# Kernel optimization log

Hardware: AMD Instinct MI355X
Metric: run time of the kernel (lower is better)

The kernel has to match this reference:

```python
import jax, jax.numpy as jnp
import numpy as np

DICT_SIZE = 512
EMBED_DIM = 64
SPARSITY = 5
COMMITMENT_COST = 0.25
EPSILON = 1e-10
COEFF_CLAMP = 1e7


def setup_inputs() -> dict:
    key = jax.random.key(0)
    kz, kd = jax.random.split(key)
    z = jax.random.normal(kz, (32, EMBED_DIM, 32, 32), dtype=jnp.float32)
    D = jax.random.normal(kd, (EMBED_DIM, DICT_SIZE), dtype=jnp.float32)
    # _normalize_dictionary(): unit L2 norm per atom (column)
    D = D / jnp.linalg.norm(D, axis=0, keepdims=True)
    return {"z": z, "dictionary": D}


def batch_omp(signals, dictionary):
    # signals: [E, N], dictionary: [E, K]
    E, N = signals.shape
    K = dictionary.shape[1]
    Dt = dictionary.T  # [K, E]
    DtD = Dt @ dictionary + EPSILON * jnp.eye(K, dtype=signals.dtype)  # [K, K]
    residual = signals
    active = jnp.zeros((N, K), dtype=bool)
    coefficients = jnp.zeros((N, K), dtype=signals.dtype)
    idx = jnp.zeros((N, 0), dtype=jnp.int32)
    rows = jnp.arange(N)
    for k in range(SPARSITY):  # small fixed unroll; active-set size is static k+1
        corr = Dt @ residual                                  # [K, N]
        corr = jnp.where(active.T, -jnp.inf, corr)
        new_atoms = jnp.argmax(corr, axis=0).astype(jnp.int32)  # [N]
        active = active.at[rows, new_atoms].set(True)
        idx = jnp.concatenate([idx, new_atoms[:, None]], axis=1)  # [N, k+1]
        G = DtD[idx[:, :, None], idx[:, None, :]]             # [N, k+1, k+1]
        y = jnp.einsum('nke,en->nk', Dt[idx], residual)       # [N, k+1]
        coeffs = jnp.linalg.solve(G, y[..., None])[..., 0]    # [N, k+1]
        update = jnp.einsum('enk,nk->en', dictionary[:, idx], coeffs)  # [E, N]
        residual = signals - update
        coefficients = coefficients.at[rows[:, None], idx].set(coeffs)
    return coefficients.T  # [K, N]


def reference(z, dictionary):
    B, E, H, W = z.shape
    # [B,E,H,W] -> [E, N]
    z_flat = z.transpose(0, 2, 3, 1).reshape(-1, E).T
    # sparse coding is done under no_grad in torch
    coefficients = jax.lax.stop_gradient(batch_omp(z_flat, dictionary))
    coefficients = jnp.clip(coefficients, -COEFF_CLAMP, COEFF_CLAMP)  # [K, N]
    z_q_flat = dictionary @ coefficients                               # [E, N]
    z_q_reshaped = z_q_flat.T.reshape(B, H, W, E).transpose(0, 3, 1, 2)
    rec_loss = jnp.mean((jax.lax.stop_gradient(z_q_flat) - z_flat) ** 2)
    commit_loss = jnp.mean((z_q_flat - jax.lax.stop_gradient(z_flat)) ** 2)
    effective_cost = COMMITMENT_COST * (1.0 + SPARSITY / 10.0)
    coeff_loss = jnp.mean(jnp.abs(coefficients))
    loss = rec_loss + effective_cost * commit_loss + 0.001 * coeff_loss
    # straight-through estimator with clamp
    z_q = z + jax.lax.stop_gradient(jnp.clip(z_q_reshaped - z, -1.0, 1.0))
    return z_q, loss, coefficients
```

## Files before the change

kernel.cpp:

```cpp
#include <hip/hip_runtime.h>
#include <math.h>

#define NSIG 32768
#define KD   512
#define ED   64
#define SP   5

__global__ __launch_bounds__(256) void k_dtd(const float* __restrict__ D,
                                             double* __restrict__ DtD) {
  int flat = blockIdx.x * 256 + threadIdx.x;
  int i = flat >> 9, j = flat & 511;
  double acc = 0.0;
  #pragma unroll
  for (int e = 0; e < ED; ++e)
    acc += (double)D[e * KD + i] * (double)D[e * KD + j];
  if (i == j) acc += 1e-10;
  DtD[flat] = acc;
}

__global__ __launch_bounds__(256) void k_zero(float4* __restrict__ p, size_t count4) {
  size_t i = (size_t)blockIdx.x * 256 + threadIdx.x;
  size_t stride = (size_t)gridDim.x * 256;
  float4 zv = make_float4(0.f, 0.f, 0.f, 0.f);
  for (; i < count4; i += stride) p[i] = zv;
}

template <int K>
__device__ __forceinline__ void omp_iter(const double* __restrict__ DtD,
                                         const double (&c0)[16], unsigned& amask,
                                         int (&idx)[SP], double (&cc)[SP],
                                         double (&tri)[15], double (&c0sel)[SP],
                                         int li) {
  double vb = -INFINITY;
  int ab = 0x7FFFFFFF;
  #pragma unroll
  for (int j4 = 0; j4 < 4; ++j4) {
    int a0 = (j4 << 7) + (li << 2);
    double v0 = c0[4 * j4], v1 = c0[4 * j4 + 1];
    double v2 = c0[4 * j4 + 2], v3 = c0[4 * j4 + 3];
    #pragma unroll
    for (int m = 0; m < K; ++m) {
      const double* gp = DtD + (size_t)idx[m] * KD + a0;
      double2 gA = *(const double2*)gp;
      double2 gB = *(const double2*)(gp + 2);
      v0 -= gA.x * cc[m];
      v1 -= gA.y * cc[m];
      v2 -= gB.x * cc[m];
      v3 -= gB.y * cc[m];
    }
    v0 = ((amask >> (4 * j4 + 0)) & 1u) ? -INFINITY : v0;
    v1 = ((amask >> (4 * j4 + 1)) & 1u) ? -INFINITY : v1;
    v2 = ((amask >> (4 * j4 + 2)) & 1u) ? -INFINITY : v2;
    v3 = ((amask >> (4 * j4 + 3)) & 1u) ? -INFINITY : v3;
    if (v0 > vb) { vb = v0; ab = a0; }
    if (v1 > vb) { vb = v1; ab = a0 + 1; }
    if (v2 > vb) { vb = v2; ab = a0 + 2; }
    if (v3 > vb) { vb = v3; ab = a0 + 3; }
  }
  #pragma unroll
  for (int s = 16; s >= 1; s >>= 1) {
    double ov = __shfl_xor(vb, s, 64);
    int    oa = __shfl_xor(ab, s, 64);
    if (ov > vb || (ov == vb && oa < ab)) { vb = ov; ab = oa; }
  }
  idx[K] = ab;
  if (((ab >> 2) & 31) == li) amask |= 1u << ((((ab >> 7) << 2)) | (ab & 3));
  const double* drow = DtD + (size_t)ab * KD;
  double bb[SP], u[SP];
  #pragma unroll
  for (int m = 0; m < K; ++m) bb[m] = drow[idx[m]];
  {
    double csel = vb;
    #pragma unroll
    for (int m = 0; m < K; ++m) csel += bb[m] * cc[m];
    c0sel[K] = csel;
  }
  double sch = drow[ab];
  #pragma unroll
  for (int i = 0; i < K; ++i) {
    double ui = 0.0;
    #pragma unroll
    for (int m = 0; m < K; ++m) {
      int lo = i < m ? i : m, hi = i < m ? m : i;
      ui += tri[lo * SP - lo * (lo + 1) / 2 + hi] * bb[m];
    }
    u[i] = ui;
    sch -= bb[i] * ui;
  }
  double r = 1.0 / sch;
  #pragma unroll
  for (int i = 0; i < K; ++i) {
    #pragma unroll
    for (int j = i; j < K; ++j) tri[i * SP - i * (i + 1) / 2 + j] += r * u[i] * u[j];
    tri[i * SP - i * (i + 1) / 2 + K] = -r * u[i];
  }
  tri[K * SP - K * (K + 1) / 2 + K] = r;
  double h[SP];
  #pragma unroll
  for (int i = 0; i <= K; ++i) {
    double s = 0.0;
    #pragma unroll
    for (int j = 0; j <= K; ++j) {
      int lo = i < j ? i : j, hi = i < j ? j : i;
      s += tri[lo * SP - lo * (lo + 1) / 2 + hi] * c0sel[j];
    }
    h[i] = s;
  }
  #pragma unroll
  for (int i = 0; i < K; ++i) cc[i] = h[i] - cc[i];
  cc[K] = h[K];
}

__device__ __forceinline__ void corr_phase(const float* __restrict__ z,
                                           const float* __restrict__ D,
                                           float* __restrict__ Dlds,
                                           float* __restrict__ zbuf,
                                           int tid, int li, int mysig,
                                           int blockId, double (&c0)[16]) {
  int n = blockId * 8 + mysig;
  int b = n >> 10, p0 = (blockId * 8) & 1023;
  {
    const float* zb = z + (size_t)b * 65536 + p0;
    #pragma unroll
    for (int k2 = 0; k2 < 2; ++k2) {
      int f = tid + 256 * k2;
      zbuf[f] = zb[(f >> 3) * 1024 + (f & 7)];
    }
  }
  #pragma unroll
  for (int j = 0; j < 16; ++j) c0[j] = 0.0;
  for (int t4 = 0; t4 < 4; ++t4) {
    __syncthreads();
    {
      const float4* src = (const float4*)(D + t4 * 16 * 512);
      float4* dst = (float4*)Dlds;
      #pragma unroll
      for (int i = 0; i < 8; ++i) dst[tid + 256 * i] = src[tid + 256 * i];
    }
    __syncthreads();
    #pragma unroll 4
    for (int e = 0; e < 16; ++e) {
      double zv = (double)zbuf[(t4 * 16 + e) * 8 + mysig];
      const float* drow = Dlds + e * 512;
      #pragma unroll
      for (int j4 = 0; j4 < 4; ++j4) {
        float4 dv = *(const float4*)(drow + (j4 << 7) + (li << 2));
        c0[4 * j4 + 0] += zv * (double)dv.x;
        c0[4 * j4 + 1] += zv * (double)dv.y;
        c0[4 * j4 + 2] += zv * (double)dv.z;
        c0[4 * j4 + 3] += zv * (double)dv.w;
      }
    }
  }
}

__global__ __launch_bounds__(256) void k_fused(const float* __restrict__ z,
                                               const float* __restrict__ D,
                                               const double* __restrict__ DtD,
                                               float* __restrict__ coefOut,
                                               int* __restrict__ idxWs,
                                               double* __restrict__ cWs,
                                               double* __restrict__ csumWs) {
  __shared__ float Dlds[16 * 512];
  __shared__ float zbuf[64 * 8];
  int tid = threadIdx.x;
  int li = tid & 31;
  int mysig = ((tid >> 6) << 1) | ((tid >> 5) & 1);
  int n = blockIdx.x * 8 + mysig;
  double c0[16];
  corr_phase(z, D, Dlds, zbuf, tid, li, mysig, blockIdx.x, c0);
  unsigned amask = 0;
  int idx[SP]; double cc[SP]; double tri[15]; double c0sel[SP];
  omp_iter<0>(DtD, c0, amask, idx, cc, tri, c0sel, li);
  omp_iter<1>(DtD, c0, amask, idx, cc, tri, c0sel, li);
  omp_iter<2>(DtD, c0, amask, idx, cc, tri, c0sel, li);
  omp_iter<3>(DtD, c0, amask, idx, cc, tri, c0sel, li);
  omp_iter<4>(DtD, c0, amask, idx, cc, tri, c0sel, li);
  if (li == 0) {
    double cs = 0.0;
    #pragma unroll
    for (int j = 0; j < SP; ++j) {
      double cj = cc[j];
      cj = fmin(fmax(cj, -10000000.0), 10000000.0);
      cs += fabs(cj);
      idxWs[n * SP + j] = idx[j];
      cWs[n * SP + j] = cj;
      coefOut[(size_t)idx[j] * NSIG + n] = (float)cj;
    }
    csumWs[n] = cs;
  }
}

__global__ __launch_bounds__(256) void k_corr_probe(const float* __restrict__ z,
                                                    const float* __restrict__ D,
                                                    double* __restrict__ probeWs) {
  __shared__ float Dlds[16 * 512];
  __shared__ float zbuf[64 * 8];
  int tid = threadIdx.x;
  int li = tid & 31;
  int mysig = ((tid >> 6) << 1) | ((tid >> 5) & 1);
  double c0[16];
  corr_phase(z, D, Dlds, zbuf, tid, li, mysig, blockIdx.x, c0);
  double s = 0.0;
  #pragma unroll
  for (int j = 0; j < 16; ++j) s += c0[j];
  if (s == 12345.6789012345) probeWs[blockIdx.x] = s;
}

__global__ __launch_bounds__(256) void k_zq(const float* __restrict__ z,
                                            const float* __restrict__ D,
                                            const int* __restrict__ idxWs,
                                            const double* __restrict__ cWs,
                                            float* __restrict__ zqOut,
                                            double* __restrict__ recWs) {
  int t = threadIdx.x;
  size_t flat = (size_t)blockIdx.x * 256 + t;
  int b = (int)(flat >> 16);
  int e = (int)((flat >> 10) & 63);
  int p = (int)(flat & 1023);
  int n = b * 1024 + p;
  double u = 0.0;
  #pragma unroll
  for (int j = 0; j < SP; ++j) {
    int a = idxWs[n * SP + j];
    u += (double)D[e * KD + a] * cWs[n * SP + j];
  }
  float zv = z[flat];
  double d = u - (double)zv;
  double dc = fmin(fmax(d, -1.0), 1.0);
  zqOut[flat] = (float)((double)zv + dc);
  __shared__ double red[256];
  red[t] = d * d;
  __syncthreads();
  #pragma unroll
  for (int s = 128; s >= 1; s >>= 1) {
    if (t < s) red[t] += red[t + s];
    __syncthreads();
  }
  if (t == 0) recWs[blockIdx.x] = red[0];
}

__global__ __launch_bounds__(256) void k_loss(const double* __restrict__ recWs,
                                              const double* __restrict__ csumWs,
                                              float* __restrict__ lossOut) {
  int t = threadIdx.x;
  double r = 0.0, c = 0.0;
  for (int i = t; i < 8192; i += 256) r += recWs[i];
  for (int i = t; i < NSIG; i += 256) c += csumWs[i];
  __shared__ double red[512];
  red[t] = r; red[256 + t] = c;
  __syncthreads();
  #pragma unroll
  for (int s = 128; s >= 1; s >>= 1) {
    if (t < s) { red[t] += red[t + s]; red[256 + t] += red[256 + t + s]; }
    __syncthreads();
  }
  if (t == 0) {
    double rec = red[0] / (double)(64.0 * 32768.0);
    double cm  = red[256] / (double)(512.0 * 32768.0);
    double loss = rec + 0.375 * rec + 0.001 * cm;
    lossOut[0] = (float)loss;
  }
}

extern "C" void kernel_launch(void* const* d_in, const int* in_sizes, int n_in,
                              void* d_out, int out_size, void* d_ws, size_t ws_size,
                              hipStream_t stream) {
  const float* z = (const float*)d_in[0];
  const float* D = (const float*)d_in[1];
  float* out = (float*)d_out;
  float* zqOut   = out;
  float* lossOut = out + 2097152;
  float* coefOut = out + 2097153;

  char* w = (char*)d_ws;
  double* DtD    = (double*)w; w += (size_t)KD * KD * 8;
  int*    idxWs  = (int*)w;    w += (size_t)NSIG * SP * 4;
  double* cWs    = (double*)w; w += (size_t)NSIG * SP * 8;
  double* csumWs = (double*)w; w += (size_t)NSIG * 8;
  double* recWs  = (double*)w; w += (size_t)8192 * 8;
  double* probeWs = (double*)w; w += (size_t)4096 * 8;

  k_dtd<<<1024, 256, 0, stream>>>(D, DtD);
  k_zero<<<2048, 256, 0, stream>>>((float4*)coefOut, (size_t)KD * NSIG / 4);
  k_fused<<<NSIG / 8, 256, 0, stream>>>(z, D, DtD, coefOut, idxWs, cWs, csumWs);
  k_zq<<<8192, 256, 0, stream>>>(z, D, idxWs, cWs, zqOut, recWs);
  k_loss<<<1, 256, 0, stream>>>(recWs, csumWs, lossOut);
  k_corr_probe<<<2048, 256, 0, stream>>>(z, D, probeWs);
}
```

Before: 263.3 us.

## Compute two signals per wave in correlation phase and drop probe kernel

The correlation phase is restructured so each 64-lane wave computes correlations for two signals at once. Each lane reads 8 contiguous dictionary atoms from LDS and reuses them for both signals, which halves LDS reads per FMA. The results are then redistributed with shuffles back into the per-half-wave layout the OMP iterations expect. The separate probe kernel that reran the correlation phase is also removed, eliminating a full extra launch's worth of work.

Result: faster. 229.3 us (-12.9%).

```diff
diff --git a/kernel.cpp b/kernel.cpp
--- a/kernel.cpp
+++ b/kernel.cpp
@@ -109,49 +109,6 @@
   #pragma unroll
   for (int i = 0; i < K; ++i) cc[i] = h[i] - cc[i];
   cc[K] = h[K];
-}
-
-__device__ __forceinline__ void corr_phase(const float* __restrict__ z,
-                                           const float* __restrict__ D,
-                                           float* __restrict__ Dlds,
-                                           float* __restrict__ zbuf,
-                                           int tid, int li, int mysig,
-                                           int blockId, double (&c0)[16]) {
-  int n = blockId * 8 + mysig;
-  int b = n >> 10, p0 = (blockId * 8) & 1023;
-  {
-    const float* zb = z + (size_t)b * 65536 + p0;
-    #pragma unroll
-    for (int k2 = 0; k2 < 2; ++k2) {
-      int f = tid + 256 * k2;
-      zbuf[f] = zb[(f >> 3) * 1024 + (f & 7)];
-    }
-  }
-  #pragma unroll
-  for (int j = 0; j < 16; ++j) c0[j] = 0.0;
-  for (int t4 = 0; t4 < 4; ++t4) {
-    __syncthreads();
-    {
-      const float4* src = (const float4*)(D + t4 * 16 * 512);
-      float4* dst = (float4*)Dlds;
-      #pragma unroll
-      for (int i = 0; i < 8; ++i) dst[tid + 256 * i] = src[tid + 256 * i];
-    }
-    __syncthreads();
-    #pragma unroll 4
-    for (int e = 0; e < 16; ++e) {
-      double zv = (double)zbuf[(t4 * 16 + e) * 8 + mysig];
-      const float* drow = Dlds + e * 512;
-      #pragma unroll
-      for (int j4 = 0; j4 < 4; ++j4) {
-        float4 dv = *(const float4*)(drow + (j4 << 7) + (li << 2));
-        c0[4 * j4 + 0] += zv * (double)dv.x;
-        c0[4 * j4 + 1] += zv * (double)dv.y;
-        c0[4 * j4 + 2] += zv * (double)dv.z;
-        c0[4 * j4 + 3] += zv * (double)dv.w;
-      }
-    }
-  }
 }
 
 __global__ __launch_bounds__(256) void k_fused(const float* __restrict__ z,
@@ -164,11 +121,67 @@
   __shared__ float Dlds[16 * 512];
   __shared__ float zbuf[64 * 8];
   int tid = threadIdx.x;
-  int li = tid & 31;
-  int mysig = ((tid >> 6) << 1) | ((tid >> 5) & 1);
-  int n = blockIdx.x * 8 + mysig;
+  int lane = tid & 63;
+  int wv = tid >> 6;
+  int li = lane & 31;
+  int g  = lane >> 5;
+  int n = blockIdx.x * 8 + 2 * wv + g;
+  {
+    int n0 = blockIdx.x * 8;
+    int b = n0 >> 10, p0 = n0 & 1023;
+    const float* zb = z + (size_t)b * 65536 + p0;
+    #pragma unroll
+    for (int k2 = 0; k2 < 2; ++k2) {
+      int f = tid + 256 * k2;
+      zbuf[f] = zb[(f >> 3) * 1024 + (f & 7)];
+    }
+  }
+  double cA[8], cB[8];
+  #pragma unroll
+  for (int p = 0; p < 8; ++p) { cA[p] = 0.0; cB[p] = 0.0; }
+  for (int t4 = 0; t4 < 4; ++t4) {
+    __syncthreads();
+    {
+      const float4* src = (const float4*)(D + t4 * 16 * 512);
+      float4* dst = (float4*)Dlds;
+      #pragma unroll
+      for (int i = 0; i < 8; ++i) dst[tid + 256 * i] = src[tid + 256 * i];
+    }
+    __syncthreads();
+    #pragma unroll 4
+    for (int e = 0; e < 16; ++e) {
+      float2 zz = *(const float2*)(zbuf + (t4 * 16 + e) * 8 + 2 * wv);
+      double zA = (double)zz.x, zB = (double)zz.y;
+      const float* dp = Dlds + e * 512 + lane * 8;
+      float4 d0 = *(const float4*)dp;
+      float4 d1 = *(const float4*)(dp + 4);
+      double dv[8] = {(double)d0.x, (double)d0.y, (double)d0.z, (double)d0.w,
+                      (double)d1.x, (double)d1.y, (double)d1.z, (double)d1.w};
+      #pragma unroll
+      for (int p = 0; p < 8; ++p) {
+        cA[p] += zA * dv[p];
+        cB[p] += zB * dv[p];
+      }
+    }
+  }
   double c0[16];
-  corr_phase(z, D, Dlds, zbuf, tid, li, mysig, blockIdx.x, c0);
+  {
+    int odd = li & 1;
+    #pragma unroll
+    for (int j4 = 0; j4 < 4; ++j4) {
+      int src = 16 * j4 + (li >> 1);
+      #pragma unroll
+      for (int bit = 0; bit < 4; ++bit) {
+        double tA0 = __shfl(cA[bit], src, 64);
+        double tA1 = __shfl(cA[4 + bit], src, 64);
+        double tB0 = __shfl(cB[bit], src, 64);
+        double tB1 = __shfl(cB[4 + bit], src, 64);
+        double vA = odd ? tA1 : tA0;
+        double vB = odd ? tB1 : tB0;
+        c0[4 * j4 + bit] = g ? vB : vA;
+      }
+    }
+  }
   unsigned amask = 0;
   int idx[SP]; double cc[SP]; double tri[15]; double c0sel[SP];
   omp_iter<0>(DtD, c0, amask, idx, cc, tri, c0sel, li);
@@ -189,22 +202,6 @@
     }
     csumWs[n] = cs;
   }
-}
-
-__global__ __launch_bounds__(256) void k_corr_probe(const float* __restrict__ z,
-                                                    const float* __restrict__ D,
-                                                    double* __restrict__ probeWs) {
-  __shared__ float Dlds[16 * 512];
-  __shared__ float zbuf[64 * 8];
-  int tid = threadIdx.x;
-  int li = tid & 31;
-  int mysig = ((tid >> 6) << 1) | ((tid >> 5) & 1);
-  double c0[16];
-  corr_phase(z, D, Dlds, zbuf, tid, li, mysig, blockIdx.x, c0);
-  double s = 0.0;
-  #pragma unroll
-  for (int j = 0; j < 16; ++j) s += c0[j];
-  if (s == 12345.6789012345) probeWs[blockIdx.x] = s;
 }
 
 __global__ __launch_bounds__(256) void k_zq(const float* __restrict__ z,
@@ -279,12 +276,10 @@
   double* cWs    = (double*)w; w += (size_t)NSIG * SP * 8;
   double* csumWs = (double*)w; w += (size_t)NSIG * 8;
   double* recWs  = (double*)w; w += (size_t)8192 * 8;
-  double* probeWs = (double*)w; w += (size_t)4096 * 8;
 
   k_dtd<<<1024, 256, 0, stream>>>(D, DtD);
   k_zero<<<2048, 256, 0, stream>>>((float4*)coefOut, (size_t)KD * NSIG / 4);
   k_fused<<<NSIG / 8, 256, 0, stream>>>(z, D, DtD, coefOut, idxWs, cWs, csumWs);
   k_zq<<<8192, 256, 0, stream>>>(z, D, idxWs, cWs, zqOut, recWs);
   k_loss<<<1, 256, 0, stream>>>(recWs, csumWs, lossOut);
-  k_corr_probe<<<2048, 256, 0, stream>>>(z, D, probeWs);
-}
+}
```
